# Kernel tuning notes

Measured on AMD Instinct MI355X. Metric: run time of the kernel, lower is better.

The kernel has to match this reference:

```python
import jax, jax.numpy as jnp
import numpy as np

N = 100000   # nodes
E = 600000   # edges
K = 3        # TAGConv hops
EPS = 1e-5   # BatchNorm eps
SLOPE = 0.01 # LeakyReLU negative slope


def setup_inputs() -> dict:
    key = jax.random.key(0)
    ks = jax.random.split(key, 8)
    y = jax.random.normal(ks[0], (N, 128), dtype=jnp.float32)
    edge_index = jax.random.randint(ks[1], (2, E), 0, N, dtype=jnp.int64)
    edge_attr = jax.random.uniform(ks[2], (E,), dtype=jnp.float32)
    # TAGConv layer l has (K+1) weight matrices [in, out]; bias only on first two layers
    W1 = 0.1 * jax.random.normal(ks[3], (K + 1, 128, 128), dtype=jnp.float32)
    b1 = jnp.full((128,), 0.1, dtype=jnp.float32)
    W2 = 0.1 * jax.random.normal(ks[4], (K + 1, 128, 128), dtype=jnp.float32)
    b2 = jnp.full((128,), 0.1, dtype=jnp.float32)
    W3 = 0.1 * jax.random.normal(ks[5], (K + 1, 128, 64), dtype=jnp.float32)
    g1 = jnp.ones((128,), jnp.float32); be1 = jnp.zeros((128,), jnp.float32)
    g2 = jnp.ones((128,), jnp.float32); be2 = jnp.zeros((128,), jnp.float32)
    g3 = jnp.ones((64,), jnp.float32);  be3 = jnp.zeros((64,), jnp.float32)
    return dict(y=y, edge_index=edge_index, edge_attr=edge_attr,
                W1=W1, b1=b1, g1=g1, be1=be1,
                W2=W2, b2=b2, g2=g2, be2=be2,
                W3=W3, g3=g3, be3=be3)


def _tag_conv(x, W, b, src, dst, norm):
    # out = sum_{k=0..K} A_hat^k x @ W_k (+ b)
    out = x @ W[0]
    h = x
    for k in range(1, W.shape[0]):
        h = jax.ops.segment_sum(norm[:, None] * h[src], dst, num_segments=N)
        out = out + h @ W[k]
    return out if b is None else out + b


def _bn(x, g, b):
    # BatchNorm1d training mode: biased batch stats over nodes
    m = x.mean(axis=0)
    v = jnp.mean((x - m) ** 2, axis=0)
    return (x - m) * jax.lax.rsqrt(v + EPS) * g + b


def reference(y, edge_index, edge_attr, W1, b1, g1, be1, W2, b2, g2, be2, W3, g3, be3):
    src, dst = edge_index[0], edge_index[1]
    # gcn_norm (symmetric, no self-loops): D^{-1/2} A D^{-1/2}
    deg = jax.ops.segment_sum(edge_attr, dst, num_segments=N)
    dis = jnp.where(deg > 0, jax.lax.rsqrt(jnp.maximum(deg, 1e-12)), 0.0)
    norm = dis[src] * edge_attr * dis[dst]
    lrelu = lambda t: jax.nn.leaky_relu(t, SLOPE)
    x = lrelu(_bn(_tag_conv(y, W1, b1, src, dst, norm), g1, be1))
    x = lrelu(_bn(_tag_conv(x, W2, b2, src, dst, norm), g2, be2))
    x = lrelu(_bn(_tag_conv(x, W3, None, src, dst, norm), g3, be3))
    return x
```

## Files before the change

### kernel.cpp

```cpp
#include <hip/hip_runtime.h>
#include <hip/hip_bf16.h>

typedef unsigned short b16;
typedef __attribute__((ext_vector_type(8))) unsigned short us8;
typedef __attribute__((ext_vector_type(8))) short short8;
typedef __attribute__((ext_vector_type(4))) float float4v;

#define NN 100000
#define NE 600000

__device__ __forceinline__ float bf2f(b16 u) {
    return __uint_as_float(((unsigned)u) << 16);
}
__device__ __forceinline__ b16 f2bf(float f) {
    unsigned x = __float_as_uint(f);
    return (b16)((x + 0x7fffu + ((x >> 16) & 1u)) >> 16);
}

__global__ void k_detect(const void* __restrict__ y, const void* __restrict__ ei,
                         int* __restrict__ flags) {
    if (threadIdx.x == 0 && blockIdx.x == 0) {
        const b16* p = (const b16*)y;
        int f32 = 0;
        for (int i = 0; i < 128; ++i) {
            float v = bf2f(p[i]);
            if (!(fabsf(v) < 1e4f)) { f32 = 1; break; }
        }
        flags[0] = f32;
        const long long* q = (const long long*)ei;
        int i64 = 1;
        for (int i = 0; i < 4; ++i) {
            long long v = q[i];
            if (v < 0 || v >= NN) i64 = 0;
        }
        flags[1] = i64;
    }
}

#define PB_B1 0
#define PB_B2 128
#define PB_G1 256
#define PB_BE1 384
#define PB_G2 512
#define PB_BE2 640
#define PB_G3 768
#define PB_BE3 832
#define PB_SZ 896

__global__ void k_cvtall(const void* b1, const void* b2, const void* g1,
                         const void* be1, const void* g2, const void* be2,
                         const void* g3, const void* be3, float* __restrict__ PB,
                         const int* __restrict__ flags) {
    int i = blockIdx.x * blockDim.x + threadIdx.x;
    if (i >= PB_SZ) return;
    const void* srcs[8] = {b1, b2, g1, be1, g2, be2, g3, be3};
    int seg, off;
    if (i < 768) { seg = i >> 7; off = seg << 7; }
    else if (i < 832) { seg = 6; off = 768; }
    else { seg = 7; off = 832; }
    int idx = i - off;
    const void* s = srcs[seg];
    PB[i] = flags[0] ? ((const float*)s)[idx] : bf2f(((const b16*)s)[idx]);
}

__global__ void k_idx(const void* __restrict__ ei, int* __restrict__ src32,
                      int* __restrict__ dst32, const int* __restrict__ flags,
                      float* __restrict__ deg, int* __restrict__ cnt) {
    int e = blockIdx.x * blockDim.x + threadIdx.x;
    if (e < NN) { deg[e] = 0.f; cnt[e] = 0; }
    if (e >= NE) return;
    int s, d;
    if (flags[1]) {
        const long long* p = (const long long*)ei;
        s = (int)p[e];
        d = (int)p[NE + e];
    } else {
        const int* p = (const int*)ei;
        s = p[e];
        d = p[NE + e];
    }
    src32[e] = ((unsigned)s < NN) ? s : 0;
    dst32[e] = ((unsigned)d < NN) ? d : 0;
}

__global__ void k_degcnt(const int* __restrict__ dst, const void* __restrict__ ea,
                         float* __restrict__ deg, int* __restrict__ cnt,
                         const int* __restrict__ flags) {
    int e = blockIdx.x * blockDim.x + threadIdx.x;
    if (e >= NE) return;
    float w = flags[0] ? ((const float*)ea)[e] : bf2f(((const b16*)ea)[e]);
    int d = dst[e];
    unsafeAtomicAdd(&deg[d], w);
    atomicAdd(&cnt[d], 1);
}

#define SCAN_B 1024
#define SCAN_NB ((NN + SCAN_B - 1) / SCAN_B)

__global__ __launch_bounds__(SCAN_B) void k_scan1(const int* __restrict__ cnt,
                                                  int* __restrict__ inc,
                                                  int* __restrict__ bsum,
                                                  float* __restrict__ deg) {
    __shared__ int s[SCAN_B];
    int i = blockIdx.x * SCAN_B + threadIdx.x;
    if (i < NN) {
        float d = deg[i];
        deg[i] = (d > 0.f) ? rsqrtf(fmaxf(d, 1e-12f)) : 0.f;
    }
    s[threadIdx.x] = (i < NN) ? cnt[i] : 0;
    __syncthreads();
    for (int off = 1; off < SCAN_B; off <<= 1) {
        int t = (threadIdx.x >= off) ? s[threadIdx.x - off] : 0;
        __syncthreads();
        s[threadIdx.x] += t;
        __syncthreads();
    }
    if (i < NN) inc[i] = s[threadIdx.x];
    if (threadIdx.x == SCAN_B - 1) bsum[blockIdx.x] = s[SCAN_B - 1];
}

__global__ void k_scan2(int* bsum) {
    int lane = threadIdx.x & 63;
    int a0 = (lane < SCAN_NB) ? bsum[lane] : 0;
    int a1 = (lane + 64 < SCAN_NB) ? bsum[lane + 64] : 0;
#pragma unroll
    for (int off = 1; off < 64; off <<= 1) {
        int t = __shfl_up(a0, off);
        if (lane >= off) a0 += t;
    }
    int tot0 = __shfl(a0, 63);
#pragma unroll
    for (int off = 1; off < 64; off <<= 1) {
        int t = __shfl_up(a1, off);
        if (lane >= off) a1 += t;
    }
    int e0 = __shfl_up(a0, 1);
    if (lane == 0) e0 = 0;
    int e1 = __shfl_up(a1, 1) + tot0;
    if (lane == 0) e1 = tot0;
    if (lane < SCAN_NB) bsum[lane] = e0;
    if (lane + 64 < SCAN_NB) bsum[lane + 64] = e1;
}

__global__ void k_scan3(const int* __restrict__ inc, const int* __restrict__ bsum,
                        int* __restrict__ rowptr, int* __restrict__ cnt) {
    int i = blockIdx.x * blockDim.x + threadIdx.x;
    if (i == 0) rowptr[0] = 0;
    if (i < NN) {
        rowptr[i + 1] = inc[i] + bsum[i / SCAN_B];
        cnt[i] = 0;
    }
}

__global__ void k_fill(const int* __restrict__ src, const int* __restrict__ dst,
                       const void* __restrict__ ea, const float* __restrict__ dis,
                       const int* __restrict__ rowptr, int* __restrict__ fill,
                       int* __restrict__ csrc, float* __restrict__ cw,
                       const int* __restrict__ flags) {
    int e = blockIdx.x * blockDim.x + threadIdx.x;
    if (e >= NE) return;
    float a = flags[0] ? ((const float*)ea)[e] : bf2f(((const b16*)ea)[e]);
    int d = dst[e];
    int s = src[e];
    int pos = rowptr[d] + atomicAdd(&fill[d], 1);
    csrc[pos] = s;
    cw[pos] = dis[s] * a * dis[d];
}

__global__ void k_pack(const void* __restrict__ W, b16* __restrict__ Wp, int NC,
                       const int* __restrict__ flags) {
    int f = blockIdx.x * blockDim.x + threadIdx.x;
    int total = 512 * NC / 8;
    if (f >= total) return;
    int lane = f & 63;
    int rest = f >> 6;
    int CT = NC >> 4;
    int ct = rest % CT, ks = rest / CT;
    int k0 = 32 * ks + (lane >> 4) * 8;
    int col = 16 * ct + (lane & 15);
    us8 v;
#pragma unroll
    for (int j = 0; j < 8; ++j) {
        float x = flags[0] ? ((const float*)W)[(size_t)(k0 + j) * NC + col]
                           : bf2f(((const b16*)W)[(size_t)(k0 + j) * NC + col]);
        v[j] = f2bf(x);
    }
    *(us8*)&Wp[(size_t)f * 8] = v;
}

__global__ void k_cast(const void* __restrict__ y, b16* __restrict__ XC,
                       const int* __restrict__ flags, float* __restrict__ gstat) {
    int i = blockIdx.x * blockDim.x + threadIdx.x;
    if (i < 768) gstat[i] = 0.f;
    if (i >= NN * 32) return;
    int row = i >> 5, cg = i & 31;
    float4 v;
    if (flags[0]) {
        v = ((const float4*)y)[i];
    } else {
        ushort4 u = ((const ushort4*)y)[i];
        v = make_float4(bf2f(u.x), bf2f(u.y), bf2f(u.z), bf2f(u.w));
    }
    ushort4 o;
    o.x = f2bf(v.x); o.y = f2bf(v.y); o.z = f2bf(v.z); o.w = f2bf(v.w);
    *(ushort4*)&XC[(size_t)row * 512 + 4 * cg] = o;
}

__global__ __launch_bounds__(256) void k_spmm(b16* __restrict__ XC, int ci, int co,
                                              const int* __restrict__ rowptr,
                                              const int* __restrict__ csrc,
                                              const float* __restrict__ cw) {
    int gid = blockIdx.x * blockDim.x + threadIdx.x;
    int node = gid >> 6;
    if (node >= NN) return;
    int lane = gid & 63;
    int grp = lane >> 4;
    int l15 = lane & 15;
    int beg = rowptr[node], end = rowptr[node + 1];

    float a0[8], a1[8];
#pragma unroll
    for (int j = 0; j < 8; ++j) {
        a0[j] = 0.f;
        a1[j] = 0.f;
    }
    for (int i = beg; i < end; i += 8) {
        int e0 = i + grp, e1 = i + 4 + grp;
        float w0 = (e0 < end) ? cw[e0] : 0.f;
        float w1 = (e1 < end) ? cw[e1] : 0.f;
        int lim = end - 1;
        int s0 = csrc[e0 < lim ? e0 : lim];
        int s1 = csrc[e1 < lim ? e1 : lim];
        us8 u0 = *(const us8*)&XC[(size_t)s0 * 512 + ci + 8 * l15];
        us8 u1 = *(const us8*)&XC[(size_t)s1 * 512 + ci + 8 * l15];
#pragma unroll
        for (int j = 0; j < 8; ++j) {
            a0[j] = fmaf(w0, bf2f(u0[j]), a0[j]);
            a1[j] = fmaf(w1, bf2f(u1[j]), a1[j]);
        }
    }
#pragma unroll
    for (int j = 0; j < 8; ++j) a0[j] += a1[j];
#pragma unroll
    for (int j = 0; j < 8; ++j) a0[j] += __shfl_xor(a0[j], 16);
#pragma unroll
    for (int j = 0; j < 8; ++j) a0[j] += __shfl_xor(a0[j], 32);
    if (grp == 0) {
        us8 o;
#pragma unroll
        for (int j = 0; j < 8; ++j) o[j] = f2bf(a0[j]);
        *(us8*)&XC[(size_t)node * 512 + co + 8 * l15] = o;
    }
}

template <int NC>
__global__ __launch_bounds__(256) void k_mgemm(const b16* __restrict__ XC,
                                               const b16* __restrict__ Wp,
                                               const float* __restrict__ bias,
                                               b16* __restrict__ OUT,
                                               float* __restrict__ gsum,
                                               float* __restrict__ gsq) {
    constexpr int CT = NC / 16;
    __shared__ float csum[NC], csq[NC];
    const int tid = threadIdx.x;
    const int wave = tid >> 6;
    const int lane = tid & 63;
    const int quad = lane >> 4;
    const int l15 = lane & 15;
    const int rbase = blockIdx.x * 128 + wave * 32;

    for (int i = tid; i < NC; i += 256) {
        csum[i] = 0.f;
        csq[i] = 0.f;
    }

    float4v acc[2][CT];
#pragma unroll
    for (int rt = 0; rt < 2; ++rt)
#pragma unroll
        for (int ct = 0; ct < CT; ++ct) acc[rt][ct] = (float4v)(0.f);

    const b16* gA[2];
#pragma unroll
    for (int rt = 0; rt < 2; ++rt) {
        int r = rbase + 16 * rt + l15;
        if (r >= NN) r = NN - 1;
        gA[rt] = XC + (size_t)r * 512 + quad * 8;
    }
    const b16* gB = Wp + lane * 8;

    short8 afc[2], bfc[CT], afn[2], bfn[CT];
#pragma unroll
    for (int rt = 0; rt < 2; ++rt) afc[rt] = *(const short8*)(gA[rt]);
#pragma unroll
    for (int ct = 0; ct < CT; ++ct) bfc[ct] = *(const short8*)(gB + ct * 512);

    for (int ks = 0; ks < 16; ++ks) {
        if (ks < 15) {
#pragma unroll
            for (int rt = 0; rt < 2; ++rt)
                afn[rt] = *(const short8*)(gA[rt] + 32 * (ks + 1));
#pragma unroll
            for (int ct = 0; ct < CT; ++ct)
                bfn[ct] = *(const short8*)(gB + (size_t)((ks + 1) * CT + ct) * 512);
        }
#pragma unroll
        for (int rt = 0; rt < 2; ++rt)
#pragma unroll
            for (int ct = 0; ct < CT; ++ct)
                acc[rt][ct] = __builtin_amdgcn_mfma_f32_16x16x32_bf16(
                    afc[rt], bfc[ct], acc[rt][ct], 0, 0, 0);
        if (ks < 15) {
#pragma unroll
            for (int rt = 0; rt < 2; ++rt) afc[rt] = afn[rt];
#pragma unroll
            for (int ct = 0; ct < CT; ++ct) bfc[ct] = bfn[ct];
        }
    }

#pragma unroll
    for (int rt = 0; rt < 2; ++rt) {
#pragma unroll
        for (int ct = 0; ct < CT; ++ct) {
            int col = 16 * ct + l15;
            float bv = bias ? bias[col] : 0.f;
            float s = 0.f, sq = 0.f;
#pragma unroll
            for (int r = 0; r < 4; ++r) {
                int row = rbase + 16 * rt + quad * 4 + r;
                if (row < NN) {
                    float v = acc[rt][ct][r] + bv;
                    OUT[(size_t)row * NC + col] = f2bf(v);
                    s += v;
                    sq += v * v;
                }
            }
            s += __shfl_xor(s, 16);
            s += __shfl_xor(s, 32);
            sq += __shfl_xor(sq, 16);
            sq += __shfl_xor(sq, 32);
            if (quad == 0) {
                atomicAdd(&csum[col], s);
                atomicAdd(&csq[col], sq);
            }
        }
    }
    __syncthreads();
    for (int i = tid; i < NC; i += 256) {
        unsafeAtomicAdd(&gsum[i], csum[i]);
        unsafeAtomicAdd(&gsq[i], csq[i]);
    }
}

__global__ void k_bnparam(const float* gsum, const float* gsq, const float* g,
                          const float* be, float* scale, float* shift, int ncols) {
    int c = threadIdx.x;
    if (c < ncols) {
        float m = gsum[c] * (1.f / NN);
        float v = gsq[c] * (1.f / NN) - m * m;
        v = fmaxf(v, 0.f);
        float s = rsqrtf(v + 1e-5f) * g[c];
        scale[c] = s;
        shift[c] = be[c] - m * s;
    }
}

__global__ void k_bnapply_mid(const b16* __restrict__ OUT,
                              const float* __restrict__ scale,
                              const float* __restrict__ shift, b16* __restrict__ XC) {
    int i = blockIdx.x * blockDim.x + threadIdx.x;
    if (i >= NN * 64) return;
    int row = i >> 6, c = (i & 63) * 2;
    ushort2 u = *(const ushort2*)&OUT[(size_t)row * 128 + c];
    float a = fmaf(bf2f(u.x), scale[c], shift[c]);
    float b = fmaf(bf2f(u.y), scale[c + 1], shift[c + 1]);
    a = a > 0.f ? a : 0.01f * a;
    b = b > 0.f ? b : 0.01f * b;
    ushort2 o;
    o.x = f2bf(a);
    o.y = f2bf(b);
    *(ushort2*)&XC[(size_t)row * 512 + c] = o;
}

__global__ void k_bnapply_last(const b16* __restrict__ OUT,
                               const float* __restrict__ scale,
                               const float* __restrict__ shift, void* __restrict__ dout,
                               const int* __restrict__ flags) {
    int i = blockIdx.x * blockDim.x + threadIdx.x;
    if (i >= NN * 64) return;
    int c = i & 63;
    float v = fmaf(bf2f(OUT[i]), scale[c], shift[c]);
    v = v > 0.f ? v : 0.01f * v;
    if (flags[0])
        ((float*)dout)[i] = v;
    else
        ((b16*)dout)[i] = f2bf(v);
}

extern "C" void kernel_launch(void* const* d_in, const int* in_sizes, int n_in,
                              void* d_out, int out_size, void* d_ws, size_t ws_size,
                              hipStream_t stream) {
    const void* y   = d_in[0];
    const void* ei  = d_in[1];
    const void* ea  = d_in[2];
    const void* W1  = d_in[3];
    const void* b1  = d_in[4];
    const void* g1  = d_in[5];
    const void* be1 = d_in[6];
    const void* W2  = d_in[7];
    const void* b2  = d_in[8];
    const void* g2  = d_in[9];
    const void* be2 = d_in[10];
    const void* W3  = d_in[11];
    const void* g3  = d_in[12];
    const void* be3 = d_in[13];

    char* w = (char*)d_ws;
    size_t used = 0;
    auto carve = [&](size_t bytes) -> char* {
        char* p = w + used;
        used += (bytes + 255) & ~(size_t)255;
        return p;
    };

    int* flags   = (int*)carve(16);
    int* src32   = (int*)carve((size_t)NE * 4);
    int* dst32   = (int*)carve((size_t)NE * 4);
    float* deg   = (float*)carve((size_t)NN * 4);
    int* cnt     = (int*)carve((size_t)NN * 4);
    int* rowptr  = (int*)carve((size_t)(NN + 1) * 4);
    int* cscan   = (int*)carve((size_t)NN * 4);
    int* bsum    = (int*)carve((size_t)SCAN_NB * 4);
    int* csrc    = (int*)carve((size_t)NE * 4);
    float* cw    = (float*)carve((size_t)NE * 4);
    float* PB    = (float*)carve(PB_SZ * 4);
    b16* Wp1     = (b16*)carve((size_t)512 * 128 * 2);
    b16* Wp2     = (b16*)carve((size_t)512 * 128 * 2);
    b16* Wp3     = (b16*)carve((size_t)512 * 64 * 2);
    b16* OUT     = (b16*)carve((size_t)NN * 128 * 2);
    float* gstat = (float*)carve(768 * 4);
    float* scale = (float*)carve(128 * 4);
    float* shift = (float*)carve(128 * 4);
    b16* XC      = (b16*)carve((size_t)NN * 512 * 2);

    k_detect<<<1, 64, 0, stream>>>(y, ei, flags);
    k_cvtall<<<(PB_SZ + 255) / 256, 256, 0, stream>>>(b1, b2, g1, be1, g2, be2, g3,
                                                      be3, PB, flags);
    k_pack<<<(512 * 128 / 8 + 255) / 256, 256, 0, stream>>>(W1, Wp1, 128, flags);
    k_pack<<<(512 * 128 / 8 + 255) / 256, 256, 0, stream>>>(W2, Wp2, 128, flags);
    k_pack<<<(512 * 64 / 8 + 255) / 256, 256, 0, stream>>>(W3, Wp3, 64, flags);

    k_idx<<<(NE + 255) / 256, 256, 0, stream>>>(ei, src32, dst32, flags, deg, cnt);
    k_degcnt<<<(NE + 255) / 256, 256, 0, stream>>>(dst32, ea, deg, cnt, flags);
    k_scan1<<<SCAN_NB, SCAN_B, 0, stream>>>(cnt, cscan, bsum, deg);
    k_scan2<<<1, 64, 0, stream>>>(bsum);
    k_scan3<<<(NN + 255) / 256, 256, 0, stream>>>(cscan, bsum, rowptr, cnt);
    k_fill<<<(NE + 255) / 256, 256, 0, stream>>>(src32, dst32, ea, deg, rowptr, cnt,
                                                 csrc, cw, flags);

    k_cast<<<(NN * 32 + 255) / 256, 256, 0, stream>>>(y, XC, flags, gstat);

    auto spmm = [&](int ci, int co) {
        k_spmm<<<(NN * 64 + 255) / 256, 256, 0, stream>>>(XC, ci, co, rowptr, csrc, cw);
    };
    const int gemm_grid = (NN + 127) / 128;

    auto layer = [&](int li, const b16* Wp, const float* bias, const float* g,
                     const float* be, int NC, bool last) {
        spmm(0, 128);
        spmm(128, 256);
        spmm(256, 384);
        float* gs = gstat + li * 256;
        float* gq = gs + 128;
        if (NC == 128)
            k_mgemm<128><<<gemm_grid, 256, 0, stream>>>(XC, Wp, bias, OUT, gs, gq);
        else
            k_mgemm<64><<<gemm_grid, 256, 0, stream>>>(XC, Wp, bias, OUT, gs, gq);
        k_bnparam<<<1, NC, 0, stream>>>(gs, gq, g, be, scale, shift, NC);
        if (last)
            k_bnapply_last<<<(NN * 64 + 255) / 256, 256, 0, stream>>>(OUT, scale, shift,
                                                                      d_out, flags);
        else
            k_bnapply_mid<<<(NN * 64 + 255) / 256, 256, 0, stream>>>(OUT, scale, shift,
                                                                     XC);
    };

    layer(0, Wp1, PB + PB_B1, PB + PB_G1, PB + PB_BE1, 128, false);
    layer(1, Wp2, PB + PB_B2, PB + PB_G2, PB + PB_BE2, 128, false);
    layer(2, Wp3, nullptr, PB + PB_G3, PB + PB_BE3, 64, true);
}
```

Before: 755.9 us.

## Pack CSR src/weight into 64-bit pairs and slice SpMM across feature columns

The CSR fill now stores each edge's source index and normalized weight as a single 64-bit pair, so the SpMM needs one load per edge instead of two. The SpMM kernel is restructured so each block handles a 16-column feature slice for 16 nodes (8 slices per row). Each wave processes 4 nodes, with 16 edges gathered in parallel at 8-byte granularity. This changes the gather pattern and lets the same edges be reread by 8 blocks. It aims to improve L2 locality of feature rows and parallelism, at the cost of narrower 8-byte gathers and repeated index loads.

```diff
diff --git a/kernel.cpp b/kernel.cpp
--- a/kernel.cpp
+++ b/kernel.cpp
@@ -155,7 +155,7 @@
 __global__ void k_fill(const int* __restrict__ src, const int* __restrict__ dst,
                        const void* __restrict__ ea, const float* __restrict__ dis,
                        const int* __restrict__ rowptr, int* __restrict__ fill,
-                       int* __restrict__ csrc, float* __restrict__ cw,
+                       unsigned long long* __restrict__ pairs,
                        const int* __restrict__ flags) {
     int e = blockIdx.x * blockDim.x + threadIdx.x;
     if (e >= NE) return;
@@ -163,8 +163,8 @@
     int d = dst[e];
     int s = src[e];
     int pos = rowptr[d] + atomicAdd(&fill[d], 1);
-    csrc[pos] = s;
-    cw[pos] = dis[s] * a * dis[d];
+    float wgt = dis[s] * a * dis[d];
+    pairs[pos] = ((unsigned long long)__float_as_uint(wgt) << 32) | (unsigned)s;
 }
 
 __global__ void k_pack(const void* __restrict__ W, b16* __restrict__ Wp, int NC,
@@ -206,50 +206,51 @@
     *(ushort4*)&XC[(size_t)row * 512 + 4 * cg] = o;
 }
 
-__global__ __launch_bounds__(256) void k_spmm(b16* __restrict__ XC, int ci, int co,
-                                              const int* __restrict__ rowptr,
-                                              const int* __restrict__ csrc,
-                                              const float* __restrict__ cw) {
-    int gid = blockIdx.x * blockDim.x + threadIdx.x;
-    int node = gid >> 6;
-    if (node >= NN) return;
-    int lane = gid & 63;
-    int grp = lane >> 4;
-    int l15 = lane & 15;
-    int beg = rowptr[node], end = rowptr[node + 1];
-
-    float a0[8], a1[8];
-#pragma unroll
-    for (int j = 0; j < 8; ++j) {
-        a0[j] = 0.f;
-        a1[j] = 0.f;
-    }
-    for (int i = beg; i < end; i += 8) {
-        int e0 = i + grp, e1 = i + 4 + grp;
-        float w0 = (e0 < end) ? cw[e0] : 0.f;
-        float w1 = (e1 < end) ? cw[e1] : 0.f;
-        int lim = end - 1;
-        int s0 = csrc[e0 < lim ? e0 : lim];
-        int s1 = csrc[e1 < lim ? e1 : lim];
-        us8 u0 = *(const us8*)&XC[(size_t)s0 * 512 + ci + 8 * l15];
-        us8 u1 = *(const us8*)&XC[(size_t)s1 * 512 + ci + 8 * l15];
-#pragma unroll
-        for (int j = 0; j < 8; ++j) {
-            a0[j] = fmaf(w0, bf2f(u0[j]), a0[j]);
-            a1[j] = fmaf(w1, bf2f(u1[j]), a1[j]);
-        }
-    }
-#pragma unroll
-    for (int j = 0; j < 8; ++j) a0[j] += a1[j];
-#pragma unroll
-    for (int j = 0; j < 8; ++j) a0[j] += __shfl_xor(a0[j], 16);
-#pragma unroll
-    for (int j = 0; j < 8; ++j) a0[j] += __shfl_xor(a0[j], 32);
-    if (grp == 0) {
-        us8 o;
-#pragma unroll
-        for (int j = 0; j < 8; ++j) o[j] = f2bf(a0[j]);
-        *(us8*)&XC[(size_t)node * 512 + co + 8 * l15] = o;
+__global__ __launch_bounds__(256) void k_spmms(b16* __restrict__ XC, int ci, int co,
+                                               const int* __restrict__ rowptr,
+                                               const unsigned long long* __restrict__ pairs) {
+    const int slice = blockIdx.x & 7;
+    const int g = blockIdx.x >> 3;
+    const int wave = threadIdx.x >> 6;
+    const int lane = threadIdx.x & 63;
+    const int slot = lane >> 2;
+    const int c4 = lane & 3;
+    const int cin = ci + slice * 16 + c4 * 4;
+    const int cout = co + slice * 16 + c4 * 4;
+    const int n0 = g * 16 + wave * 4;
+
+#pragma unroll
+    for (int k = 0; k < 4; ++k) {
+        int node = n0 + k;
+        int beg = rowptr[node], end = rowptr[node + 1];
+        float a[4] = {0.f, 0.f, 0.f, 0.f};
+        for (int i = beg; i < end; i += 16) {
+            int e = i + slot;
+            int lim = end - 1;
+            unsigned long long p = pairs[e < lim ? e : lim];
+            float w = (e < end) ? __uint_as_float((unsigned)(p >> 32)) : 0.f;
+            int s = (int)(p & 0xffffffffu);
+            ushort4 u = *(const ushort4*)&XC[(size_t)s * 512 + cin];
+            a[0] = fmaf(w, bf2f(u.x), a[0]);
+            a[1] = fmaf(w, bf2f(u.y), a[1]);
+            a[2] = fmaf(w, bf2f(u.z), a[2]);
+            a[3] = fmaf(w, bf2f(u.w), a[3]);
+        }
+#pragma unroll
+        for (int j = 0; j < 4; ++j) {
+            a[j] += __shfl_xor(a[j], 4);
+            a[j] += __shfl_xor(a[j], 8);
+            a[j] += __shfl_xor(a[j], 16);
+            a[j] += __shfl_xor(a[j], 32);
+        }
+        if (slot == 0) {
+            ushort4 o;
+            o.x = f2bf(a[0]);
+            o.y = f2bf(a[1]);
+            o.z = f2bf(a[2]);
+            o.w = f2bf(a[3]);
+            *(ushort4*)&XC[(size_t)node * 512 + cout] = o;
+        }
     }
 }
 
@@ -431,8 +432,7 @@
     int* rowptr  = (int*)carve((size_t)(NN + 1) * 4);
     int* cscan   = (int*)carve((size_t)NN * 4);
     int* bsum    = (int*)carve((size_t)SCAN_NB * 4);
-    int* csrc    = (int*)carve((size_t)NE * 4);
-    float* cw    = (float*)carve((size_t)NE * 4);
+    unsigned long long* pairs = (unsigned long long*)carve((size_t)NE * 8);
     float* PB    = (float*)carve(PB_SZ * 4);
     b16* Wp1     = (b16*)carve((size_t)512 * 128 * 2);
     b16* Wp2     = (b16*)carve((size_t)512 * 128 * 2);
@@ -456,12 +456,13 @@
     k_scan2<<<1, 64, 0, stream>>>(bsum);
     k_scan3<<<(NN + 255) / 256, 256, 0, stream>>>(cscan, bsum, rowptr, cnt);
     k_fill<<<(NE + 255) / 256, 256, 0, stream>>>(src32, dst32, ea, deg, rowptr, cnt,
-                                                 csrc, cw, flags);
+                                                 pairs, flags);
 
     k_cast<<<(NN * 32 + 255) / 256, 256, 0, stream>>>(y, XC, flags, gstat);
 
+    const int SPMM_GRID = 8 * (NN / 16);
     auto spmm = [&](int ci, int co) {
-        k_spmm<<<(NN * 64 + 255) / 256, 256, 0, stream>>>(XC, ci, co, rowptr, csrc, cw);
+        k_spmms<<<SPMM_GRID, 256, 0, stream>>>(XC, ci, co, rowptr, pairs);
     };
     const int gemm_grid = (NN + 127) / 128;
 
```

Result: slower. 1.834 ms (+142.6%).

## Reassociate last layer as Horner form and pack CSR index/weight pairs

Applied to the files above, without the earlier changes.

The last TAGConv layer is rewritten in Horner form. The input is first projected to 64 columns per hop with a single GEMM (Z = X·[W0..W3]), and the three sparse propagations then run on 64-wide data, each adding the next Z slice, instead of propagating 128-wide features. Batch statistics for that layer come from a separate reduction kernel. CSR source indices and edge weights are also packed into one 64-bit array so each edge needs one load. This halves the gather traffic in the last layer's SpMMs, at the cost of an extra Z buffer, an extra stats pass, and different bf16 rounding from the reordered accumulation.

```diff
diff --git a/kernel.cpp b/kernel.cpp
--- a/kernel.cpp
+++ b/kernel.cpp
@@ -155,7 +155,7 @@
 __global__ void k_fill(const int* __restrict__ src, const int* __restrict__ dst,
                        const void* __restrict__ ea, const float* __restrict__ dis,
                        const int* __restrict__ rowptr, int* __restrict__ fill,
-                       int* __restrict__ csrc, float* __restrict__ cw,
+                       unsigned long long* __restrict__ pairs,
                        const int* __restrict__ flags) {
     int e = blockIdx.x * blockDim.x + threadIdx.x;
     if (e >= NE) return;
@@ -163,8 +163,8 @@
     int d = dst[e];
     int s = src[e];
     int pos = rowptr[d] + atomicAdd(&fill[d], 1);
-    csrc[pos] = s;
-    cw[pos] = dis[s] * a * dis[d];
+    float wgt = dis[s] * a * dis[d];
+    pairs[pos] = ((unsigned long long)__float_as_uint(wgt) << 32) | (unsigned)s;
 }
 
 __global__ void k_pack(const void* __restrict__ W, b16* __restrict__ Wp, int NC,
@@ -188,6 +188,26 @@
     *(us8*)&Wp[(size_t)f * 8] = v;
 }
 
+__global__ void k_pack3(const void* __restrict__ W, b16* __restrict__ Bp,
+                        const int* __restrict__ flags) {
+    int f = blockIdx.x * blockDim.x + threadIdx.x;
+    if (f >= 4096) return;
+    int lane = f & 63;
+    int rest = f >> 6;
+    int ct = rest & 15, ks = rest >> 4;
+    int k0 = 32 * ks + (lane >> 4) * 8;
+    int cp = 16 * ct + (lane & 15);
+    int km = cp >> 6, c = cp & 63;
+    us8 v;
+#pragma unroll
+    for (int j = 0; j < 8; ++j) {
+        size_t idx = (size_t)(km * 128 + k0 + j) * 64 + c;
+        float x = flags[0] ? ((const float*)W)[idx] : bf2f(((const b16*)W)[idx]);
+        v[j] = f2bf(x);
+    }
+    *(us8*)&Bp[(size_t)f * 8] = v;
+}
+
 __global__ void k_cast(const void* __restrict__ y, b16* __restrict__ XC,
                        const int* __restrict__ flags, float* __restrict__ gstat) {
     int i = blockIdx.x * blockDim.x + threadIdx.x;
@@ -208,8 +228,7 @@
 
 __global__ __launch_bounds__(256) void k_spmm(b16* __restrict__ XC, int ci, int co,
                                               const int* __restrict__ rowptr,
-                                              const int* __restrict__ csrc,
-                                              const float* __restrict__ cw) {
+                                              const unsigned long long* __restrict__ pairs) {
     int gid = blockIdx.x * blockDim.x + threadIdx.x;
     int node = gid >> 6;
     if (node >= NN) return;
@@ -225,12 +244,14 @@
         a1[j] = 0.f;
     }
     for (int i = beg; i < end; i += 8) {
-        int e0 = i + grp, e1 = i + 4 + grp;
-        float w0 = (e0 < end) ? cw[e0] : 0.f;
-        float w1 = (e1 < end) ? cw[e1] : 0.f;
+        int e0 = i + grp, e1 = e0 + 4;
         int lim = end - 1;
-        int s0 = csrc[e0 < lim ? e0 : lim];
-        int s1 = csrc[e1 < lim ? e1 : lim];
+        unsigned long long p0 = pairs[e0 < lim ? e0 : lim];
+        unsigned long long p1 = pairs[e1 < lim ? e1 : lim];
+        float w0 = (e0 < end) ? __uint_as_float((unsigned)(p0 >> 32)) : 0.f;
+        float w1 = (e1 < end) ? __uint_as_float((unsigned)(p1 >> 32)) : 0.f;
+        int s0 = (int)(p0 & 0xffffffffu);
+        int s1 = (int)(p1 & 0xffffffffu);
         us8 u0 = *(const us8*)&XC[(size_t)s0 * 512 + ci + 8 * l15];
         us8 u1 = *(const us8*)&XC[(size_t)s1 * 512 + ci + 8 * l15];
 #pragma unroll
@@ -250,6 +271,62 @@
 #pragma unroll
         for (int j = 0; j < 8; ++j) o[j] = f2bf(a0[j]);
         *(us8*)&XC[(size_t)node * 512 + co + 8 * l15] = o;
+    }
+}
+
+__global__ __launch_bounds__(256) void k_spmm64(const b16* __restrict__ G, int gstride,
+                                                int gcol, const b16* __restrict__ Z,
+                                                int zoff, b16* __restrict__ D,
+                                                const int* __restrict__ rowptr,
+                                                const unsigned long long* __restrict__ pairs) {
+    int gid = blockIdx.x * blockDim.x + threadIdx.x;
+    int node = gid >> 6;
+    if (node >= NN) return;
+    int lane = gid & 63;
+    int grp = lane >> 4;
+    int l15 = lane & 15;
+    int beg = rowptr[node], end = rowptr[node + 1];
+
+    float a0[4], a1[4];
+#pragma unroll
+    for (int j = 0; j < 4; ++j) {
+        a0[j] = 0.f;
+        a1[j] = 0.f;
+    }
+    for (int i = beg; i < end; i += 8) {
+        int e0 = i + grp, e1 = e0 + 4;
+        int lim = end - 1;
+        unsigned long long p0 = pairs[e0 < lim ? e0 : lim];
+        unsigned long long p1 = pairs[e1 < lim ? e1 : lim];
+        float w0 = (e0 < end) ? __uint_as_float((unsigned)(p0 >> 32)) : 0.f;
+        float w1 = (e1 < end) ? __uint_as_float((unsigned)(p1 >> 32)) : 0.f;
+        int s0 = (int)(p0 & 0xffffffffu);
+        int s1 = (int)(p1 & 0xffffffffu);
+        ushort4 u0 = *(const ushort4*)&G[(size_t)s0 * gstride + gcol + 4 * l15];
+        ushort4 u1 = *(const ushort4*)&G[(size_t)s1 * gstride + gcol + 4 * l15];
+        a0[0] = fmaf(w0, bf2f(u0.x), a0[0]);
+        a0[1] = fmaf(w0, bf2f(u0.y), a0[1]);
+        a0[2] = fmaf(w0, bf2f(u0.z), a0[2]);
+        a0[3] = fmaf(w0, bf2f(u0.w), a0[3]);
+        a1[0] = fmaf(w1, bf2f(u1.x), a1[0]);
+        a1[1] = fmaf(w1, bf2f(u1.y), a1[1]);
+        a1[2] = fmaf(w1, bf2f(u1.z), a1[2]);
+        a1[3] = fmaf(w1, bf2f(u1.w), a1[3]);
+    }
+#pragma unroll
+    for (int j = 0; j < 4; ++j) a0[j] += a1[j];
+#pragma unroll
+    for (int j = 0; j < 4; ++j) a0[j] += __shfl_xor(a0[j], 16);
+#pragma unroll
+    for (int j = 0; j < 4; ++j) a0[j] += __shfl_xor(a0[j], 32);
+    if (grp == 0) {
+        ushort4 z = *(const ushort4*)&Z[(size_t)node * 256 + zoff + 4 * l15];
+        ushort4 o;
+        o.x = f2bf(a0[0] + bf2f(z.x));
+        o.y = f2bf(a0[1] + bf2f(z.y));
+        o.z = f2bf(a0[2] + bf2f(z.z));
+        o.w = f2bf(a0[3] + bf2f(z.w));
+        *(ushort4*)&D[(size_t)node * 64 + 4 * l15] = o;
     }
 }
 
@@ -352,6 +429,96 @@
     }
 }
 
+__global__ __launch_bounds__(256) void k_zgemm(const b16* __restrict__ XC,
+                                               const b16* __restrict__ Bp,
+                                               b16* __restrict__ Z) {
+    const int tid = threadIdx.x;
+    const int wave = tid >> 6;
+    const int lane = tid & 63;
+    const int quad = lane >> 4;
+    const int l15 = lane & 15;
+    const int wr = wave >> 1;
+    const int wc = wave & 1;
+    const int rbase = blockIdx.x * 64 + wr * 32;
+
+    float4v acc[2][8];
+#pragma unroll
+    for (int rt = 0; rt < 2; ++rt)
+#pragma unroll
+        for (int ct = 0; ct < 8; ++ct) acc[rt][ct] = (float4v)(0.f);
+
+    const b16* gA[2];
+#pragma unroll
+    for (int rt = 0; rt < 2; ++rt) {
+        int r = rbase + 16 * rt + l15;
+        if (r >= NN) r = NN - 1;
+        gA[rt] = XC + (size_t)r * 512 + quad * 8;
+    }
+    const b16* gB = Bp + ((size_t)(wc * 8) * 64 + lane) * 8;
+
+    short8 afc[2], bfc[8], afn[2], bfn[8];
+#pragma unroll
+    for (int rt = 0; rt < 2; ++rt) afc[rt] = *(const short8*)(gA[rt]);
+#pragma unroll
+    for (int ct = 0; ct < 8; ++ct) bfc[ct] = *(const short8*)(gB + ct * 512);
+
+    for (int ks = 0; ks < 4; ++ks) {
+        if (ks < 3) {
+#pragma unroll
+            for (int rt = 0; rt < 2; ++rt)
+                afn[rt] = *(const short8*)(gA[rt] + 32 * (ks + 1));
+#pragma unroll
+            for (int ct = 0; ct < 8; ++ct)
+                bfn[ct] = *(const short8*)(gB + (size_t)((ks + 1) * 16 + ct) * 512);
+        }
+#pragma unroll
+        for (int rt = 0; rt < 2; ++rt)
+#pragma unroll
+            for (int ct = 0; ct < 8; ++ct)
+                acc[rt][ct] = __builtin_amdgcn_mfma_f32_16x16x32_bf16(
+                    afc[rt], bfc[ct], acc[rt][ct], 0, 0, 0);
+        if (ks < 3) {
+#pragma unroll
+            for (int rt = 0; rt < 2; ++rt) afc[rt] = afn[rt];
+#pragma unroll
+            for (int ct = 0; ct < 8; ++ct) bfc[ct] = bfn[ct];
+        }
+    }
+
+#pragma unroll
+    for (int rt = 0; rt < 2; ++rt) {
+#pragma unroll
+        for (int ct = 0; ct < 8; ++ct) {
+            int col = 16 * (wc * 8 + ct) + l15;
+#pragma unroll
+            for (int r = 0; r < 4; ++r) {
+                int row = rbase + 16 * rt + quad * 4 + r;
+                if (row < NN) Z[(size_t)row * 256 + col] = f2bf(acc[rt][ct][r]);
+            }
+        }
+    }
+}
+
+__global__ __launch_bounds__(256) void k_stat64(const b16* __restrict__ T,
+                                                float* __restrict__ gsum,
+                                                float* __restrict__ gsq) {
+    __shared__ float cs[64], cq[64];
+    int tid = threadIdx.x;
+    if (tid < 64) { cs[tid] = 0.f; cq[tid] = 0.f; }
+    __syncthreads();
+    for (int i = blockIdx.x * 256 + tid; i < NN * 64; i += gridDim.x * 256) {
+        float v = bf2f(T[i]);
+        int c = i & 63;
+        atomicAdd(&cs[c], v);
+        atomicAdd(&cq[c], v * v);
+    }
+    __syncthreads();
+    if (tid < 64) {
+        unsafeAtomicAdd(&gsum[tid], cs[tid]);
+        unsafeAtomicAdd(&gsq[tid], cq[tid]);
+    }
+}
+
 __global__ void k_bnparam(const float* gsum, const float* gsq, const float* g,
                           const float* be, float* scale, float* shift, int ncols) {
     int c = threadIdx.x;
@@ -382,14 +549,14 @@
     *(ushort2*)&XC[(size_t)row * 512 + c] = o;
 }
 
-__global__ void k_bnapply_last(const b16* __restrict__ OUT,
+__global__ void k_bnapply_last(const b16* __restrict__ T,
                                const float* __restrict__ scale,
                                const float* __restrict__ shift, void* __restrict__ dout,
                                const int* __restrict__ flags) {
     int i = blockIdx.x * blockDim.x + threadIdx.x;
     if (i >= NN * 64) return;
     int c = i & 63;
-    float v = fmaf(bf2f(OUT[i]), scale[c], shift[c]);
+    float v = fmaf(bf2f(T[i]), scale[c], shift[c]);
     v = v > 0.f ? v : 0.01f * v;
     if (flags[0])
         ((float*)dout)[i] = v;
@@ -431,24 +598,26 @@
     int* rowptr  = (int*)carve((size_t)(NN + 1) * 4);
     int* cscan   = (int*)carve((size_t)NN * 4);
     int* bsum    = (int*)carve((size_t)SCAN_NB * 4);
-    int* csrc    = (int*)carve((size_t)NE * 4);
-    float* cw    = (float*)carve((size_t)NE * 4);
+    unsigned long long* pairs = (unsigned long long*)carve((size_t)NE * 8);
     float* PB    = (float*)carve(PB_SZ * 4);
     b16* Wp1     = (b16*)carve((size_t)512 * 128 * 2);
     b16* Wp2     = (b16*)carve((size_t)512 * 128 * 2);
-    b16* Wp3     = (b16*)carve((size_t)512 * 64 * 2);
+    b16* Wp3c    = (b16*)carve((size_t)128 * 256 * 2);
     b16* OUT     = (b16*)carve((size_t)NN * 128 * 2);
     float* gstat = (float*)carve(768 * 4);
     float* scale = (float*)carve(128 * 4);
     float* shift = (float*)carve(128 * 4);
     b16* XC      = (b16*)carve((size_t)NN * 512 * 2);
+    b16* Z       = (b16*)carve((size_t)NN * 256 * 2);
+    b16* T0      = (b16*)carve((size_t)NN * 64 * 2);
+    b16* T1      = (b16*)carve((size_t)NN * 64 * 2);
 
     k_detect<<<1, 64, 0, stream>>>(y, ei, flags);
     k_cvtall<<<(PB_SZ + 255) / 256, 256, 0, stream>>>(b1, b2, g1, be1, g2, be2, g3,
                                                       be3, PB, flags);
     k_pack<<<(512 * 128 / 8 + 255) / 256, 256, 0, stream>>>(W1, Wp1, 128, flags);
     k_pack<<<(512 * 128 / 8 + 255) / 256, 256, 0, stream>>>(W2, Wp2, 128, flags);
-    k_pack<<<(512 * 64 / 8 + 255) / 256, 256, 0, stream>>>(W3, Wp3, 64, flags);
+    k_pack3<<<16, 256, 0, stream>>>(W3, Wp3c, flags);
 
     k_idx<<<(NE + 255) / 256, 256, 0, stream>>>(ei, src32, dst32, flags, deg, cnt);
     k_degcnt<<<(NE + 255) / 256, 256, 0, stream>>>(dst32, ea, deg, cnt, flags);
@@ -456,36 +625,38 @@
     k_scan2<<<1, 64, 0, stream>>>(bsum);
     k_scan3<<<(NN + 255) / 256, 256, 0, stream>>>(cscan, bsum, rowptr, cnt);
     k_fill<<<(NE + 255) / 256, 256, 0, stream>>>(src32, dst32, ea, deg, rowptr, cnt,
-                                                 csrc, cw, flags);
+                                                 pairs, flags);
 
     k_cast<<<(NN * 32 + 255) / 256, 256, 0, stream>>>(y, XC, flags, gstat);
 
+    const int spmm_grid = (NN * 64 + 255) / 256;
     auto spmm = [&](int ci, int co) {
-        k_spmm<<<(NN * 64 + 255) / 256, 256, 0, stream>>>(XC, ci, co, rowptr, csrc, cw);
+        k_spmm<<<spmm_grid, 256, 0, stream>>>(XC, ci, co, rowptr, pairs);
     };
     const int gemm_grid = (NN + 127) / 128;
 
-    auto layer = [&](int li, const b16* Wp, const float* bias, const float* g,
-                     const float* be, int NC, bool last) {
+    auto layer12 = [&](int li, const b16* Wp, const float* bias, const float* g,
+                       const float* be) {
         spmm(0, 128);
         spmm(128, 256);
         spmm(256, 384);
         float* gs = gstat + li * 256;
         float* gq = gs + 128;
-        if (NC == 128)
-            k_mgemm<128><<<gemm_grid, 256, 0, stream>>>(XC, Wp, bias, OUT, gs, gq);
-        else
-            k_mgemm<64><<<gemm_grid, 256, 0, stream>>>(XC, Wp, bias, OUT, gs, gq);
-        k_bnparam<<<1, NC, 0, stream>>>(gs, gq, g, be, scale, shift, NC);
-        if (last)
-            k_bnapply_last<<<(NN * 64 + 255) / 256, 256, 0, stream>>>(OUT, scale, shift,
-                                                                      d_out, flags);
-        else
-            k_bnapply_mid<<<(NN * 64 + 255) / 256, 256, 0, stream>>>(OUT, scale, shift,
-                                                                     XC);
+        k_mgemm<128><<<gemm_grid, 256, 0, stream>>>(XC, Wp, bias, OUT, gs, gq);
+        k_bnparam<<<1, 128, 0, stream>>>(gs, gq, g, be, scale, shift, 128);
+        k_bnapply_mid<<<(NN * 64 + 255) / 256, 256, 0, stream>>>(OUT, scale, shift, XC);
     };
-
-    layer(0, Wp1, PB + PB_B1, PB + PB_G1, PB + PB_BE1, 128, false);
-    layer(1, Wp2, PB + PB_B2, PB + PB_G2, PB + PB_BE2, 128, false);
-    layer(2, Wp3, nullptr, PB + PB_G3, PB + PB_BE3, 64, true);
-}
+    layer12(0, Wp1, PB + PB_B1, PB + PB_G1, PB + PB_BE1);
+    layer12(1, Wp2, PB + PB_B2, PB + PB_G2, PB + PB_BE2);
+
+    k_zgemm<<<(NN + 63) / 64, 256, 0, stream>>>(XC, Wp3c, Z);
+    k_spmm64<<<spmm_grid, 256, 0, stream>>>(Z, 256, 192, Z, 128, T0, rowptr, pairs);
+    k_spmm64<<<spmm_grid, 256, 0, stream>>>(T0, 64, 0, Z, 64, T1, rowptr, pairs);
+    k_spmm64<<<spmm_grid, 256, 0, stream>>>(T1, 64, 0, Z, 0, T0, rowptr, pairs);
+    float* gs3 = gstat + 512;
+    float* gq3 = gstat + 640;
+    k_stat64<<<256, 256, 0, stream>>>(T0, gs3, gq3);
+    k_bnparam<<<1, 64, 0, stream>>>(gs3, gq3, PB + PB_G3, PB + PB_BE3, scale, shift, 64);
+    k_bnapply_last<<<(NN * 64 + 255) / 256, 256, 0, stream>>>(T0, scale, shift, d_out,
+                                                              flags);
+}
```

After: 783.7 us. +3.7%, slower.
